# Optimization experiments

Measured on AMD Instinct MI355X. Metric: run time of the kernel, lower is better.

Reference implementation:

```python
import jax, jax.numpy as jnp
import numpy as np

EMBED_DIM = 1024
HEAD_DIM = 128

def setup_inputs() -> dict:
    key = jax.random.key(0)
    ks = jax.random.split(key, 7)
    B, S = 4, 2048
    x = jax.random.normal(ks[0], (B, S, EMBED_DIM), dtype=jnp.float32)
    # Linear params: weight [embed_dim, head_dim] (applied as x @ W + b), scaled init
    scale = 1.0 / np.sqrt(EMBED_DIM)
    Wq = jax.random.normal(ks[1], (EMBED_DIM, HEAD_DIM), dtype=jnp.float32) * scale
    Wk = jax.random.normal(ks[2], (EMBED_DIM, HEAD_DIM), dtype=jnp.float32) * scale
    Wv = jax.random.normal(ks[3], (EMBED_DIM, HEAD_DIM), dtype=jnp.float32) * scale
    bq = jax.random.normal(ks[4], (HEAD_DIM,), dtype=jnp.float32) * 0.01
    bk = jax.random.normal(ks[5], (HEAD_DIM,), dtype=jnp.float32) * 0.01
    bv = jax.random.normal(ks[6], (HEAD_DIM,), dtype=jnp.float32) * 0.01
    return {"x": x, "Wq": Wq, "bq": bq, "Wk": Wk, "bk": bk, "Wv": Wv, "bv": bv}

def reference(x, Wq, bq, Wk, bk, Wv, bv):
    # x: [B, S, E]
    S = x.shape[1]
    norm = jnp.asarray(HEAD_DIM ** 0.5, x.dtype)
    q = x @ Wq + bq  # [B, S, D]
    k = x @ Wk + bk
    v = x @ Wv + bv
    scores = jnp.einsum('bsd,btd->bst', q, k) / norm  # [B, S, S]
    causal = jnp.tril(jnp.ones((S, S), dtype=bool))
    scores = jnp.where(causal, scores, -jnp.inf)
    att = jax.nn.softmax(scores, axis=-1)
    return jnp.einsum('bst,btd->bsd', att, v)  # [B, S, D]
```

## Files before the change

kernel.cpp:

```cpp
#include <hip/hip_runtime.h>
#include <hip/hip_bf16.h>

typedef __attribute__((ext_vector_type(8))) short short8;
typedef __attribute__((ext_vector_type(4))) float f32x4;

static __device__ __forceinline__ unsigned short f2bf(float f){
  union { float f; unsigned int u; } v; v.f = f;
  unsigned int r = v.u + 0x7fffu + ((v.u >> 16) & 1u);
  return (unsigned short)(r >> 16);
}

static __device__ __forceinline__ void load_lds16(const unsigned short* g, unsigned short* l){
  __builtin_amdgcn_global_load_lds(
      (const __attribute__((address_space(1))) unsigned int*)(g),
      (__attribute__((address_space(3))) unsigned int*)(l), 16, 0, 0);
}

__global__ void k_prep(const float* __restrict__ x, unsigned short* __restrict__ xb,
                       const float* __restrict__ Wq, const float* __restrict__ Wk,
                       const float* __restrict__ Wv,
                       const float* __restrict__ bq, const float* __restrict__ bk,
                       const float* __restrict__ bv,
                       unsigned short* __restrict__ Wt, float* __restrict__ bias){
  int bx = blockIdx.x;
  int tid = threadIdx.x;
  if (bx < 4096){
    int i = (bx * 256 + tid) * 8;
    float4 a = *(const float4*)(x + i);
    float4 b = *(const float4*)(x + i + 4);
    unsigned short h[8];
    h[0]=f2bf(a.x); h[1]=f2bf(a.y); h[2]=f2bf(a.z); h[3]=f2bf(a.w);
    h[4]=f2bf(b.x); h[5]=f2bf(b.y); h[6]=f2bf(b.z); h[7]=f2bf(b.w);
    *(uint4*)(xb + i) = *(uint4*)h;
  } else {
    int gid = (bx - 4096) * 256 + tid;
    int p = gid >> 17;
    int rem = gid & 131071;
    int d = rem >> 10, e = rem & 1023;
    const float* W = (p==0) ? Wq : ((p==1) ? Wk : Wv);
    Wt[gid] = f2bf(W[e*128 + d]);
    if (gid < 384){
      int pp = gid >> 7, dd = gid & 127;
      bias[gid] = (pp==0) ? bq[dd] : ((pp==1) ? bk[dd] : bv[dd]);
    }
  }
}

__global__ __launch_bounds__(256) void k_gemm_qkv(
    const unsigned short* __restrict__ Xb, const unsigned short* __restrict__ Wt,
    const float* __restrict__ bias,
    unsigned short* __restrict__ Qsw, unsigned short* __restrict__ Ksw,
    unsigned short* __restrict__ Vsw){
  __shared__ __align__(16) char smem[32768];
  unsigned short* As = (unsigned short*)smem;
  unsigned short* Bs = (unsigned short*)(smem + 8192);
  float* Lf = (float*)smem;
  int tid = threadIdx.x;
  int mt = blockIdx.x;
  int p  = blockIdx.y;
  int m0 = mt * 64;
  int w = tid >> 6, lane = tid & 63, quad = lane >> 4, l16 = lane & 15;
  int wm = (w >> 1) * 32, wn = (w & 1) * 64;
  f32x4 acc[2][4];
  #pragma unroll
  for (int i=0;i<2;i++)
    #pragma unroll
    for (int j=0;j<4;j++) acc[i][j] = (f32x4){0.f,0.f,0.f,0.f};

  const unsigned short* Wp = Wt + p * (128*1024);
  const unsigned short* Ag = Xb + (m0 + w*16 + (lane>>3))*1024 + (lane&7)*8;
  const unsigned short* Bg = Wp + (w*32 + (lane>>3))*1024 + (lane&7)*8;
  unsigned short* Al = As + (w*16)*64;
  unsigned short* Bl = Bs + (w*32)*64;

  for (int k0 = 0; k0 < 1024; k0 += 64){
    #pragma unroll
    for (int s8=0; s8<2; s8++)
      load_lds16(Ag + k0 + s8*8192, Al + s8*512);
    #pragma unroll
    for (int s8=0; s8<4; s8++)
      load_lds16(Bg + k0 + s8*8192, Bl + s8*512);
    __syncthreads();
    #pragma unroll
    for (int kk=0; kk<64; kk+=32){
      short8 af[2], bf[4];
      #pragma unroll
      for (int i=0;i<2;i++) af[i] = *(const short8*)(As + (wm + i*16 + l16)*64 + kk + quad*8);
      #pragma unroll
      for (int j=0;j<4;j++) bf[j] = *(const short8*)(Bs + (wn + j*16 + l16)*64 + kk + quad*8);
      #pragma unroll
      for (int i=0;i<2;i++)
        #pragma unroll
        for (int j=0;j<4;j++)
          acc[i][j] = __builtin_amdgcn_mfma_f32_16x16x32_bf16(af[i], bf[j], acc[i][j], 0,0,0);
    }
    __syncthreads();
  }

  const float qscale = 0.08838834764831845f;
  if (p == 2){
    #pragma unroll
    for (int i=0;i<2;i++)
      #pragma unroll
      for (int j=0;j<4;j++){
        int grow0 = m0 + wm + i*16 + quad*4;
        int col = wn + j*16 + l16;
        unsigned short pk[4];
        float bv_ = bias[256 + col];
        #pragma unroll
        for (int r=0;r<4;r++) pk[r] = f2bf(acc[i][j][r] + bv_);
        int bb2 = grow0 >> 11, s = grow0 & 2047;
        int t64 = s >> 6, srem = s & 63;
        int kc2 = srem >> 5, q2 = (srem >> 3) & 3, jj = srem & 7;
        int nt = col >> 4, l2 = col & 15;
        *(uint2*)(Vsw + (bb2*32+t64)*8192 + nt*1024 + kc2*512 + q2*128 + l2*8 + jj) = *(uint2*)pk;
      }
  } else {
    #pragma unroll
    for (int i=0;i<2;i++)
      #pragma unroll
      for (int j=0;j<4;j++)
        #pragma unroll
        for (int r=0;r<4;r++)
          Lf[(wm + i*16 + quad*4 + r)*128 + wn + j*16 + l16] = acc[i][j][r];
    __syncthreads();
    unsigned short* dst = (p==0)? Qsw : Ksw;
    float scale = (p==0)? qscale : 1.0f;
    #pragma unroll
    for (int it=0; it<8; it++){
      int g = it*256 + tid;
      int row = g >> 5, cs = (g & 31)*4;
      f32x4 a = *(const f32x4*)(Lf + row*128 + cs);
      int grow = m0 + row;
      int rt = grow >> 4, m = grow & 15;
      int kc = cs >> 5, q2 = (cs >> 3) & 3, jj = cs & 7;
      unsigned short pk[4];
      #pragma unroll
      for (int k=0;k<4;k++) pk[k] = f2bf((a[k] + bias[p*128+cs+k])*scale);
      *(uint2*)(dst + rt*2048 + kc*512 + q2*128 + m*8 + jj) = *(uint2*)pk;
    }
  }
}

__global__ __launch_bounds__(64) void k_attn(
    const unsigned short* __restrict__ Qsw, const unsigned short* __restrict__ Ksw,
    const unsigned short* __restrict__ Vsw, float* __restrict__ Apart){
  __shared__ __align__(16) unsigned short Pw[2*16*80];
  int x = blockIdx.x;
  int b = x & 3;
  int t = x >> 2;
  int c = t & 7;
  int qb = 63 - (t >> 3);
  int T32 = (qb >> 1) + 1;
  int nch = (T32 + 3) >> 2;
  if (c >= nch) return;
  int lane = threadIdx.x;
  int quad = lane >> 4, l16 = lane & 15;
  int q0 = qb * 32;

  short8 aq[2][4];
  #pragma unroll
  for (int s=0;s<2;s++)
    #pragma unroll
    for (int kc=0;kc<4;kc++)
      aq[s][kc] = *(const short8*)(Qsw + (b*128 + qb*2 + s)*2048 + kc*512 + lane*8);

  f32x4 o[2][8];
  #pragma unroll
  for (int s=0;s<2;s++)
    #pragma unroll
    for (int i=0;i<8;i++) o[s][i] = (f32x4){0.f,0.f,0.f,0.f};
  float mcol[2] = {-1e30f,-1e30f};
  float lcol[2] = {0.f,0.f};
  short8 ap[2][2];

  const unsigned short* Kb = Ksw + b*128*2048;
  const unsigned short* Vb = Vsw + b*32*8192;

  int tEnd = (T32 < c*4+4) ? T32 : (c*4+4);
  for (int tt = c*4; tt < tEnd; tt++){
    int t0 = tt * 64;
    f32x4 sc[2][4];
    #pragma unroll
    for (int s=0;s<2;s++)
      #pragma unroll
      for (int nt=0;nt<4;nt++) sc[s][nt] = (f32x4){0.f,0.f,0.f,0.f};
    __builtin_amdgcn_s_setprio(1);
    #pragma unroll
    for (int nt=0;nt<4;nt++){
      const unsigned short* Kt = Kb + ((t0>>4)+nt)*2048 + lane*8;
      #pragma unroll
      for (int kc=0;kc<4;kc++){
        short8 kf = *(const short8*)(Kt + kc*512);
        sc[0][nt] = __builtin_amdgcn_mfma_f32_16x16x32_bf16(kf, aq[0][kc], sc[0][nt], 0,0,0);
        sc[1][nt] = __builtin_amdgcn_mfma_f32_16x16x32_bf16(kf, aq[1][kc], sc[1][nt], 0,0,0);
      }
    }
    __builtin_amdgcn_s_setprio(0);
    #pragma unroll
    for (int s=0;s<2;s++){
      int qs = q0 + s*16;
      if (t0 + 63 > qs){
        #pragma unroll
        for (int nt=0;nt<4;nt++){
          int kb_ = t0 + nt*16 + quad*4;
          #pragma unroll
          for (int r=0;r<4;r++)
            if (kb_ + r > qs + l16) sc[s][nt][r] = -1e30f;
        }
      }
      float mt_ = -1e30f;
      #pragma unroll
      for (int nt=0;nt<4;nt++)
        #pragma unroll
        for (int r=0;r<4;r++) mt_ = fmaxf(mt_, sc[s][nt][r]);
      mt_ = fmaxf(mt_, __shfl_xor(mt_, 16));
      mt_ = fmaxf(mt_, __shfl_xor(mt_, 32));
      float mn = fmaxf(mcol[s], mt_);
      float al = __expf(mcol[s] - mn);
      mcol[s] = mn;
      float ls = 0.f;
      #pragma unroll
      for (int nt=0;nt<4;nt++)
        #pragma unroll
        for (int r=0;r<4;r++){
          float pv = __expf(sc[s][nt][r] - mn);
          sc[s][nt][r] = pv;
          ls += pv;
        }
      ls += __shfl_xor(ls, 16);
      ls += __shfl_xor(ls, 32);
      lcol[s] = lcol[s]*al + ls;
      #pragma unroll
      for (int r=0;r<4;r++){
        float ar = __shfl(al, quad*4 + r);
        #pragma unroll
        for (int nt=0;nt<8;nt++) o[s][nt][r] *= ar;
      }
      unsigned short* Pws = Pw + s*1280;
      #pragma unroll
      for (int nt=0;nt<4;nt++){
        unsigned short pk[4];
        #pragma unroll
        for (int r=0;r<4;r++) pk[r] = f2bf(sc[s][nt][r]);
        *(uint2*)(Pws + l16*80 + nt*16 + quad*4) = *(uint2*)pk;
      }
      ap[s][0] = *(const short8*)(Pws + l16*80 + quad*8);
      ap[s][1] = *(const short8*)(Pws + l16*80 + 32 + quad*8);
    }
    const unsigned short* Vt0 = Vb + (t0>>6)*8192 + lane*8;
    __builtin_amdgcn_s_setprio(1);
    #pragma unroll
    for (int nt=0; nt<8; nt++)
      #pragma unroll
      for (int kc2=0;kc2<2;kc2++){
        short8 vf = *(const short8*)(Vt0 + nt*1024 + kc2*512);
        o[0][nt] = __builtin_amdgcn_mfma_f32_16x16x32_bf16(ap[0][kc2], vf, o[0][nt], 0,0,0);
        o[1][nt] = __builtin_amdgcn_mfma_f32_16x16x32_bf16(ap[1][kc2], vf, o[1][nt], 0,0,0);
      }
    __builtin_amdgcn_s_setprio(0);
  }

  float* slot = Apart + (size_t)(((b*64 + qb)*8 + c)) * 4160;
  #pragma unroll
  for (int s=0;s<2;s++){
    #pragma unroll
    for (int nt=0;nt<8;nt++)
      #pragma unroll
      for (int r=0;r<4;r++)
        slot[(s*16 + quad*4 + r)*128 + nt*16 + l16] = o[s][nt][r];
    if (quad == 0){
      slot[4096 + s*16 + l16] = mcol[s];
      slot[4128 + s*16 + l16] = lcol[s];
    }
  }
}

__global__ __launch_bounds__(256) void k_acomb(const float* __restrict__ Apart,
                                               float* __restrict__ out){
  int b = blockIdx.x & 3, qb = blockIdx.x >> 2;
  int T32 = (qb >> 1) + 1;
  int nch = (T32 + 3) >> 2;
  const float* base = Apart + (size_t)((b*64 + qb)*8) * 4160;
  int tid = threadIdx.x;
  int row = tid >> 3;
  int c0 = (tid & 7) * 16;
  float m = -1e30f;
  for (int c=0;c<nch;c++) m = fmaxf(m, base[c*4160 + 4096 + row]);
  f32x4 acc[4];
  #pragma unroll
  for (int g=0;g<4;g++) acc[g] = (f32x4){0.f,0.f,0.f,0.f};
  float lsum = 0.f;
  for (int c=0;c<nch;c++){
    float e = __expf(base[c*4160 + 4096 + row] - m);
    lsum += base[c*4160 + 4128 + row] * e;
    #pragma unroll
    for (int g=0;g<4;g++){
      f32x4 v = *(const f32x4*)(base + c*4160 + row*128 + c0 + g*4);
      acc[g] += v * e;
    }
  }
  float inv = 1.0f / lsum;
  float* op = out + (size_t)(b*2048 + qb*32 + row)*128 + c0;
  #pragma unroll
  for (int g=0;g<4;g++){
    f32x4 r = acc[g] * inv;
    *(f32x4*)(op + g*4) = r;
  }
}

extern "C" void kernel_launch(void* const* d_in, const int* in_sizes, int n_in,
                              void* d_out, int out_size, void* d_ws, size_t ws_size,
                              hipStream_t stream) {
  const float* x  = (const float*)d_in[0];
  const float* Wq = (const float*)d_in[1];
  const float* bq = (const float*)d_in[2];
  const float* Wk = (const float*)d_in[3];
  const float* bk = (const float*)d_in[4];
  const float* Wv = (const float*)d_in[5];
  const float* bv = (const float*)d_in[6];
  char* ws = (char*)d_ws;
  unsigned short* Xb   = (unsigned short*)(ws);
  unsigned short* Wt   = (unsigned short*)(ws + 16777216);
  float*          bias = (float*)(ws + 17563648);
  unsigned short* Qsw  = (unsigned short*)(ws + 17565184);
  unsigned short* Ksw  = (unsigned short*)(ws + 19662336);
  unsigned short* Vsw  = (unsigned short*)(ws + 21759488);
  float*          Apart= (float*)(ws + 23856640);
  float* out = (float*)d_out;

  hipLaunchKernelGGL(k_prep,    dim3(5632),    dim3(256), 0, stream,
                     x, Xb, Wq, Wk, Wv, bq, bk, bv, Wt, bias);
  hipLaunchKernelGGL(k_gemm_qkv,dim3(128,3),   dim3(256), 0, stream,
                     Xb, Wt, bias, Qsw, Ksw, Vsw);
  hipLaunchKernelGGL(k_attn,    dim3(2048),    dim3(64),  0, stream, Qsw, Ksw, Vsw, Apart);
  hipLaunchKernelGGL(k_acomb,   dim3(256),     dim3(256), 0, stream, Apart, out);
}
```

Baseline: 137.3 us.

## Double-buffer QKV GEMM LDS and split attention into 16-row query blocks

The QKV projection GEMM now double-buffers its LDS tiles, issuing the next k-slice's global-to-LDS loads before computing the current one. This removes one barrier per iteration and lets load latency overlap with MFMA work. The attention kernel processes one 16-row query tile per wave instead of two, with up to 16 key chunks of 128 keys each, giving 4x more blocks and a finer causal split. In exchange, every K/V fragment is loaded twice as often per query row, and the combine kernel handles twice as many blocks.

```diff
diff --git a/kernel.cpp b/kernel.cpp
--- a/kernel.cpp
+++ b/kernel.cpp
@@ -51,9 +51,7 @@
     const float* __restrict__ bias,
     unsigned short* __restrict__ Qsw, unsigned short* __restrict__ Ksw,
     unsigned short* __restrict__ Vsw){
-  __shared__ __align__(16) char smem[32768];
-  unsigned short* As = (unsigned short*)smem;
-  unsigned short* Bs = (unsigned short*)(smem + 8192);
+  __shared__ __align__(16) char smem[49152];
   float* Lf = (float*)smem;
   int tid = threadIdx.x;
   int mt = blockIdx.x;
@@ -70,24 +68,32 @@
   const unsigned short* Wp = Wt + p * (128*1024);
   const unsigned short* Ag = Xb + (m0 + w*16 + (lane>>3))*1024 + (lane&7)*8;
   const unsigned short* Bg = Wp + (w*32 + (lane>>3))*1024 + (lane&7)*8;
-  unsigned short* Al = As + (w*16)*64;
-  unsigned short* Bl = Bs + (w*32)*64;
-
-  for (int k0 = 0; k0 < 1024; k0 += 64){
-    #pragma unroll
-    for (int s8=0; s8<2; s8++)
-      load_lds16(Ag + k0 + s8*8192, Al + s8*512);
-    #pragma unroll
-    for (int s8=0; s8<4; s8++)
-      load_lds16(Bg + k0 + s8*8192, Bl + s8*512);
-    __syncthreads();
+  int aoff = (w*16)*64;
+  int boff = (w*32)*64;
+
+  auto stage = [&](int sel, int k0){
+    unsigned short* Al = (unsigned short*)(smem + sel*24576) + aoff;
+    unsigned short* Bl = (unsigned short*)(smem + sel*24576 + 8192) + boff;
+    load_lds16(Ag + k0, Al);
+    load_lds16(Ag + k0 + 8192, Al + 512);
+    #pragma unroll
+    for (int s8=0; s8<4; s8++) load_lds16(Bg + k0 + s8*8192, Bl + s8*512);
+  };
+
+  stage(0, 0);
+  __syncthreads();
+  int cur = 0;
+  for (int t=0; t<16; t++){
+    if (t < 15) stage(cur^1, (t+1)*64);
+    const unsigned short* Ac = (const unsigned short*)(smem + cur*24576);
+    const unsigned short* Bc = Ac + 4096;
     #pragma unroll
     for (int kk=0; kk<64; kk+=32){
       short8 af[2], bf[4];
       #pragma unroll
-      for (int i=0;i<2;i++) af[i] = *(const short8*)(As + (wm + i*16 + l16)*64 + kk + quad*8);
-      #pragma unroll
-      for (int j=0;j<4;j++) bf[j] = *(const short8*)(Bs + (wn + j*16 + l16)*64 + kk + quad*8);
+      for (int i=0;i<2;i++) af[i] = *(const short8*)(Ac + (wm + i*16 + l16)*64 + kk + quad*8);
+      #pragma unroll
+      for (int j=0;j<4;j++) bf[j] = *(const short8*)(Bc + (wn + j*16 + l16)*64 + kk + quad*8);
       #pragma unroll
       for (int i=0;i<2;i++)
         #pragma unroll
@@ -95,6 +101,7 @@
           acc[i][j] = __builtin_amdgcn_mfma_f32_16x16x32_bf16(af[i], bf[j], acc[i][j], 0,0,0);
     }
     __syncthreads();
+    cur ^= 1;
   }
 
   const float qscale = 0.08838834764831845f;
@@ -145,46 +152,40 @@
 __global__ __launch_bounds__(64) void k_attn(
     const unsigned short* __restrict__ Qsw, const unsigned short* __restrict__ Ksw,
     const unsigned short* __restrict__ Vsw, float* __restrict__ Apart){
-  __shared__ __align__(16) unsigned short Pw[2*16*80];
+  __shared__ __align__(16) unsigned short Pw[16*80];
   int x = blockIdx.x;
   int b = x & 3;
   int t = x >> 2;
-  int c = t & 7;
-  int qb = 63 - (t >> 3);
-  int T32 = (qb >> 1) + 1;
-  int nch = (T32 + 3) >> 2;
+  int c = t & 15;
+  int qb = 127 - (t >> 4);
+  int T64 = (qb >> 2) + 1;
+  int nch = (T64 + 1) >> 1;
   if (c >= nch) return;
   int lane = threadIdx.x;
   int quad = lane >> 4, l16 = lane & 15;
-  int q0 = qb * 32;
-
-  short8 aq[2][4];
-  #pragma unroll
-  for (int s=0;s<2;s++)
-    #pragma unroll
-    for (int kc=0;kc<4;kc++)
-      aq[s][kc] = *(const short8*)(Qsw + (b*128 + qb*2 + s)*2048 + kc*512 + lane*8);
-
-  f32x4 o[2][8];
-  #pragma unroll
-  for (int s=0;s<2;s++)
-    #pragma unroll
-    for (int i=0;i<8;i++) o[s][i] = (f32x4){0.f,0.f,0.f,0.f};
-  float mcol[2] = {-1e30f,-1e30f};
-  float lcol[2] = {0.f,0.f};
-  short8 ap[2][2];
+  int qs = qb * 16;
+
+  short8 aq[4];
+  #pragma unroll
+  for (int kc=0;kc<4;kc++)
+    aq[kc] = *(const short8*)(Qsw + (b*128 + qb)*2048 + kc*512 + lane*8);
+
+  f32x4 o[8];
+  #pragma unroll
+  for (int i=0;i<8;i++) o[i] = (f32x4){0.f,0.f,0.f,0.f};
+  float mcol = -1e30f;
+  float lcol = 0.f;
+  short8 ap[2];
 
   const unsigned short* Kb = Ksw + b*128*2048;
   const unsigned short* Vb = Vsw + b*32*8192;
 
-  int tEnd = (T32 < c*4+4) ? T32 : (c*4+4);
-  for (int tt = c*4; tt < tEnd; tt++){
+  int tEnd = (T64 < c*2+2) ? T64 : (c*2+2);
+  for (int tt = c*2; tt < tEnd; tt++){
     int t0 = tt * 64;
-    f32x4 sc[2][4];
-    #pragma unroll
-    for (int s=0;s<2;s++)
-      #pragma unroll
-      for (int nt=0;nt<4;nt++) sc[s][nt] = (f32x4){0.f,0.f,0.f,0.f};
+    f32x4 sc[4];
+    #pragma unroll
+    for (int nt=0;nt<4;nt++) sc[nt] = (f32x4){0.f,0.f,0.f,0.f};
     __builtin_amdgcn_s_setprio(1);
     #pragma unroll
     for (int nt=0;nt<4;nt++){
@@ -192,62 +193,56 @@
       #pragma unroll
       for (int kc=0;kc<4;kc++){
         short8 kf = *(const short8*)(Kt + kc*512);
-        sc[0][nt] = __builtin_amdgcn_mfma_f32_16x16x32_bf16(kf, aq[0][kc], sc[0][nt], 0,0,0);
-        sc[1][nt] = __builtin_amdgcn_mfma_f32_16x16x32_bf16(kf, aq[1][kc], sc[1][nt], 0,0,0);
+        sc[nt] = __builtin_amdgcn_mfma_f32_16x16x32_bf16(kf, aq[kc], sc[nt], 0,0,0);
       }
     }
     __builtin_amdgcn_s_setprio(0);
-    #pragma unroll
-    for (int s=0;s<2;s++){
-      int qs = q0 + s*16;
-      if (t0 + 63 > qs){
+    if (t0 + 63 > qs){
+      #pragma unroll
+      for (int nt=0;nt<4;nt++){
+        int kb_ = t0 + nt*16 + quad*4;
         #pragma unroll
-        for (int nt=0;nt<4;nt++){
-          int kb_ = t0 + nt*16 + quad*4;
-          #pragma unroll
-          for (int r=0;r<4;r++)
-            if (kb_ + r > qs + l16) sc[s][nt][r] = -1e30f;
-        }
-      }
-      float mt_ = -1e30f;
-      #pragma unroll
-      for (int nt=0;nt<4;nt++)
-        #pragma unroll
-        for (int r=0;r<4;r++) mt_ = fmaxf(mt_, sc[s][nt][r]);
-      mt_ = fmaxf(mt_, __shfl_xor(mt_, 16));
-      mt_ = fmaxf(mt_, __shfl_xor(mt_, 32));
-      float mn = fmaxf(mcol[s], mt_);
-      float al = __expf(mcol[s] - mn);
-      mcol[s] = mn;
-      float ls = 0.f;
-      #pragma unroll
-      for (int nt=0;nt<4;nt++)
-        #pragma unroll
-        for (int r=0;r<4;r++){
-          float pv = __expf(sc[s][nt][r] - mn);
-          sc[s][nt][r] = pv;
-          ls += pv;
-        }
-      ls += __shfl_xor(ls, 16);
-      ls += __shfl_xor(ls, 32);
-      lcol[s] = lcol[s]*al + ls;
+        for (int r=0;r<4;r++)
+          if (kb_ + r > qs + l16) sc[nt][r] = -1e30f;
+      }
+    }
+    float mt_ = -1e30f;
+    #pragma unroll
+    for (int nt=0;nt<4;nt++)
+      #pragma unroll
+      for (int r=0;r<4;r++) mt_ = fmaxf(mt_, sc[nt][r]);
+    mt_ = fmaxf(mt_, __shfl_xor(mt_, 16));
+    mt_ = fmaxf(mt_, __shfl_xor(mt_, 32));
+    float mn = fmaxf(mcol, mt_);
+    float al = __expf(mcol - mn);
+    mcol = mn;
+    float ls = 0.f;
+    #pragma unroll
+    for (int nt=0;nt<4;nt++)
       #pragma unroll
       for (int r=0;r<4;r++){
-        float ar = __shfl(al, quad*4 + r);
-        #pragma unroll
-        for (int nt=0;nt<8;nt++) o[s][nt][r] *= ar;
-      }
-      unsigned short* Pws = Pw + s*1280;
-      #pragma unroll
-      for (int nt=0;nt<4;nt++){
-        unsigned short pk[4];
-        #pragma unroll
-        for (int r=0;r<4;r++) pk[r] = f2bf(sc[s][nt][r]);
-        *(uint2*)(Pws + l16*80 + nt*16 + quad*4) = *(uint2*)pk;
-      }
-      ap[s][0] = *(const short8*)(Pws + l16*80 + quad*8);
-      ap[s][1] = *(const short8*)(Pws + l16*80 + 32 + quad*8);
-    }
+        float pv = __expf(sc[nt][r] - mn);
+        sc[nt][r] = pv;
+        ls += pv;
+      }
+    ls += __shfl_xor(ls, 16);
+    ls += __shfl_xor(ls, 32);
+    lcol = lcol*al + ls;
+    #pragma unroll
+    for (int r=0;r<4;r++){
+      float ar = __shfl(al, quad*4 + r);
+      #pragma unroll
+      for (int nt=0;nt<8;nt++) o[nt][r] *= ar;
+    }
+    #pragma unroll
+    for (int nt=0;nt<4;nt++){
+      unsigned short pk[4];
+      #pragma unroll
+      for (int r=0;r<4;r++) pk[r] = f2bf(sc[nt][r]);
+      *(uint2*)(Pw + l16*80 + nt*16 + quad*4) = *(uint2*)pk;
+    }
+    ap[0] = *(const short8*)(Pw + l16*80 + quad*8);
+    ap[1] = *(const short8*)(Pw + l16*80 + 32 + quad*8);
     const unsigned short* Vt0 = Vb + (t0>>6)*8192 + lane*8;
     __builtin_amdgcn_s_setprio(1);
     #pragma unroll
@@ -255,55 +250,51 @@
       #pragma unroll
       for (int kc2=0;kc2<2;kc2++){
         short8 vf = *(const short8*)(Vt0 + nt*1024 + kc2*512);
-        o[0][nt] = __builtin_amdgcn_mfma_f32_16x16x32_bf16(ap[0][kc2], vf, o[0][nt], 0,0,0);
-        o[1][nt] = __builtin_amdgcn_mfma_f32_16x16x32_bf16(ap[1][kc2], vf, o[1][nt], 0,0,0);
+        o[nt] = __builtin_amdgcn_mfma_f32_16x16x32_bf16(ap[kc2], vf, o[nt], 0,0,0);
       }
     __builtin_amdgcn_s_setprio(0);
   }
 
-  float* slot = Apart + (size_t)(((b*64 + qb)*8 + c)) * 4160;
-  #pragma unroll
-  for (int s=0;s<2;s++){
-    #pragma unroll
-    for (int nt=0;nt<8;nt++)
-      #pragma unroll
-      for (int r=0;r<4;r++)
-        slot[(s*16 + quad*4 + r)*128 + nt*16 + l16] = o[s][nt][r];
-    if (quad == 0){
-      slot[4096 + s*16 + l16] = mcol[s];
-      slot[4128 + s*16 + l16] = lcol[s];
-    }
+  float* slot = Apart + (size_t)((b*128 + qb)*16 + c) * 2080;
+  #pragma unroll
+  for (int nt=0;nt<8;nt++)
+    #pragma unroll
+    for (int r=0;r<4;r++)
+      slot[(quad*4 + r)*128 + nt*16 + l16] = o[nt][r];
+  if (quad == 0){
+    slot[2048 + l16] = mcol;
+    slot[2064 + l16] = lcol;
   }
 }
 
 __global__ __launch_bounds__(256) void k_acomb(const float* __restrict__ Apart,
                                                float* __restrict__ out){
   int b = blockIdx.x & 3, qb = blockIdx.x >> 2;
-  int T32 = (qb >> 1) + 1;
-  int nch = (T32 + 3) >> 2;
-  const float* base = Apart + (size_t)((b*64 + qb)*8) * 4160;
+  int T64 = (qb >> 2) + 1;
+  int nch = (T64 + 1) >> 1;
+  const float* base = Apart + (size_t)((b*128 + qb)*16) * 2080;
   int tid = threadIdx.x;
-  int row = tid >> 3;
-  int c0 = (tid & 7) * 16;
+  int row = tid >> 4;
+  int c0 = (tid & 15) * 8;
   float m = -1e30f;
-  for (int c=0;c<nch;c++) m = fmaxf(m, base[c*4160 + 4096 + row]);
-  f32x4 acc[4];
-  #pragma unroll
-  for (int g=0;g<4;g++) acc[g] = (f32x4){0.f,0.f,0.f,0.f};
+  for (int c=0;c<nch;c++) m = fmaxf(m, base[c*2080 + 2048 + row]);
+  f32x4 acc[2];
+  #pragma unroll
+  for (int g=0;g<2;g++) acc[g] = (f32x4){0.f,0.f,0.f,0.f};
   float lsum = 0.f;
   for (int c=0;c<nch;c++){
-    float e = __expf(base[c*4160 + 4096 + row] - m);
-    lsum += base[c*4160 + 4128 + row] * e;
-    #pragma unroll
-    for (int g=0;g<4;g++){
-      f32x4 v = *(const f32x4*)(base + c*4160 + row*128 + c0 + g*4);
+    float e = __expf(base[c*2080 + 2048 + row] - m);
+    lsum += base[c*2080 + 2064 + row] * e;
+    #pragma unroll
+    for (int g=0;g<2;g++){
+      f32x4 v = *(const f32x4*)(base + c*2080 + row*128 + c0 + g*4);
       acc[g] += v * e;
     }
   }
   float inv = 1.0f / lsum;
-  float* op = out + (size_t)(b*2048 + qb*32 + row)*128 + c0;
-  #pragma unroll
-  for (int g=0;g<4;g++){
+  float* op = out + (size_t)(b*2048 + qb*16 + row)*128 + c0;
+  #pragma unroll
+  for (int g=0;g<2;g++){
     f32x4 r = acc[g] * inv;
     *(f32x4*)(op + g*4) = r;
   }
@@ -333,6 +324,6 @@
                      x, Xb, Wq, Wk, Wv, bq, bk, bv, Wt, bias);
   hipLaunchKernelGGL(k_gemm_qkv,dim3(128,3),   dim3(256), 0, stream,
                      Xb, Wt, bias, Qsw, Ksw, Vsw);
-  hipLaunchKernelGGL(k_attn,    dim3(2048),    dim3(64),  0, stream, Qsw, Ksw, Vsw, Apart);
-  hipLaunchKernelGGL(k_acomb,   dim3(256),     dim3(256), 0, stream, Apart, out);
-}
+  hipLaunchKernelGGL(k_attn,    dim3(8192),    dim3(64),  0, stream, Qsw, Ksw, Vsw, Apart);
+  hipLaunchKernelGGL(k_acomb,   dim3(512),     dim3(256), 0, stream, Apart, out);
+}
```

Result: no change. 136.8 us (-0.4%).
